# Optimization experiments

Hardware: AMD Instinct MI355X
Metric: run time of the kernel (lower is better)

Reference implementation:

```python
import jax, jax.numpy as jnp
import numpy as np

K = 3       # strip kernel taps
G = 2       # groups
PAD = (K - 1) // 2  # dilation=1


def setup_inputs() -> dict:
    key = jax.random.key(0)
    k1, k2, k3, k4, k5 = jax.random.split(key, 5)
    n, c, h, w = 8, 96, 256, 256
    x = jax.random.normal(k1, (n, c, h, w), dtype=jnp.float32)
    Wconv = jax.random.normal(k2, (G * K, c), dtype=jnp.float32) * 0.1   # 1x1 conv weight
    inside_all = jax.random.normal(k3, (c, 1, 1), dtype=jnp.float32) * 0.1
    lamb_l = jax.random.normal(k4, (c,), dtype=jnp.float32) * 0.1
    lamb_h = jax.random.normal(k5, (c,), dtype=jnp.float32) * 0.1
    return {"x": x, "Wconv": Wconv, "inside_all": inside_all,
            "lamb_l": lamb_l, "lamb_h": lamb_h}


def reference(x, Wconv, inside_all, lamb_l, lamb_h):
    n, c, h, w = x.shape
    cg = c // G
    # dynamic per-(sample, group) filter from global average pool + 1x1 conv + tanh
    m = x.mean(axis=(2, 3))                       # (n, c)
    filt = jnp.tanh(m @ Wconv.T).reshape(n, G, K)  # (n, G, K)
    # reflection pad along width (H=True -> horizontal strip)
    xp = jnp.pad(x, ((0, 0), (0, 0), (0, 0), (PAD, PAD)), mode="reflect")
    xr = xp.reshape(n, G, cg, h, w + 2 * PAD)
    # sliding-window multiply-accumulate over K taps (no unfold materialization)
    out = xr[..., 0:w] * filt[:, :, None, None, None, 0]
    for i in range(1, K):
        out = out + xr[..., i:i + w] * filt[:, :, None, None, None, i]
    out = out.reshape(n, c, h, w)
    # gated low/high residual mix; gap averages over width for H=True
    gap = x.mean(axis=3, keepdims=True)            # (n, c, h, 1)
    out_low = (out * (inside_all + 1.0) - inside_all * gap) * lamb_l[None, :, None, None]
    out_high = x * (lamb_h[None, :, None, None] + 1.0)
    return out_low + out_high
```

## Files before the change

kernel.cpp:

```cpp
#include <hip/hip_runtime.h>
#include <math.h>

#define NN 8
#define CC 96
#define HH 256
#define WW 256
#define GG 2
#define KK 3
#define CG (CC / GG)
#define HWD (HH * WW)

typedef float fvec4 __attribute__((ext_vector_type(4)));

__global__ __launch_bounds__(256) void mean_kernel(const float* __restrict__ x,
                                                   float* __restrict__ m) {
    const int b = blockIdx.x;
    const fvec4* xp = (const fvec4*)(x + (size_t)b * HWD);
    const int t = threadIdx.x;
    float s = 0.f;
#pragma unroll
    for (int i = 0; i < HWD / 4 / 256; ++i) {
        fvec4 v = xp[i * 256 + t];
        s += (v.x + v.y) + (v.z + v.w);
    }
#pragma unroll
    for (int off = 32; off; off >>= 1) s += __shfl_down(s, off, 64);
    __shared__ float ls[4];
    const int wid = t >> 6;
    if ((t & 63) == 0) ls[wid] = s;
    __syncthreads();
    if (t == 0) {
        float tot = (ls[0] + ls[1]) + (ls[2] + ls[3]);
        m[b] = tot * (1.0f / (float)HWD);
    }
}

__global__ void filt_kernel(const float* __restrict__ m,
                            const float* __restrict__ Wconv,
                            float* __restrict__ filt) {
    const int t = threadIdx.x;
    if (t >= NN * GG * KK) return;
    const int n = t / (GG * KK);
    const int gk = t % (GG * KK);
    float s = 0.f;
#pragma unroll
    for (int c = 0; c < CC; ++c) s += m[n * CC + c] * Wconv[gk * CC + c];
    filt[t] = tanhf(s);
}

__global__ __launch_bounds__(256) void main_kernel(
    const float* __restrict__ x, const float* __restrict__ filt,
    const float* __restrict__ inside_all, const float* __restrict__ lamb_l,
    const float* __restrict__ lamb_h, float* __restrict__ out) {
    const int wave = threadIdx.x >> 6;
    const int lane = threadIdx.x & 63;
    const int nc = blockIdx.x >> 6;
    const int row_in_nc = ((blockIdx.x & 63) << 2) + wave;
    const int c = nc % CC;
    const int n = nc / CC;
    const int g = c / CG;

    const float* fr = filt + (n * GG + g) * KK;
    const float f0 = fr[0], f1 = fr[1], f2 = fr[2];
    const float ia = inside_all[c];
    const float ll = lamb_l[c];
    const float lh1 = lamb_h[c] + 1.0f;

    const size_t base = ((size_t)nc * HH + row_in_nc) * WW;
    fvec4 v = ((const fvec4*)(x + base))[lane];

    float s = (v.x + v.y) + (v.z + v.w);
#pragma unroll
    for (int off = 1; off < 64; off <<= 1) s += __shfl_xor(s, off, 64);
    const float gap = s * (1.0f / (float)WW);

    const float left = __shfl_up(v.w, 1, 64);
    const float right = __shfl_down(v.x, 1, 64);
    const float xm1 = (lane == 0) ? v.y : left;
    const float xp1 = (lane == 63) ? v.z : right;

    const float c0 = f0 * xm1 + f1 * v.x + f2 * v.y;
    const float c1 = f0 * v.x + f1 * v.y + f2 * v.z;
    const float c2 = f0 * v.y + f1 * v.z + f2 * v.w;
    const float c3 = f0 * v.z + f1 * v.w + f2 * xp1;

    const float a = ia + 1.0f;
    const float bterm = ia * gap;

    fvec4 o;
    o.x = (c0 * a - bterm) * ll + v.x * lh1;
    o.y = (c1 * a - bterm) * ll + v.y * lh1;
    o.z = (c2 * a - bterm) * ll + v.z * lh1;
    o.w = (c3 * a - bterm) * ll + v.w * lh1;
    __builtin_nontemporal_store(o, (fvec4*)(out + base) + lane);
}

extern "C" void kernel_launch(void* const* d_in, const int* in_sizes, int n_in,
                              void* d_out, int out_size, void* d_ws,
                              size_t ws_size, hipStream_t stream) {
    const float* x = (const float*)d_in[0];
    const float* Wconv = (const float*)d_in[1];
    const float* inside_all = (const float*)d_in[2];
    const float* lamb_l = (const float*)d_in[3];
    const float* lamb_h = (const float*)d_in[4];
    float* out = (float*)d_out;

    float* m = (float*)d_ws;
    float* filt = m + NN * CC;

    mean_kernel<<<NN * CC, 256, 0, stream>>>(x, m);
    filt_kernel<<<1, 64, 0, stream>>>(m, Wconv, filt);
    main_kernel<<<(NN * CC * HH) / 4, 256, 0, stream>>>(x, filt, inside_all,
                                                        lamb_l, lamb_h, out);
}
```

Before: 92.68 us.

## Fuse mean, filter, and strip conv into one cooperative grid-synced kernel

Replaces the three-kernel sequence with a single cooperative kernel, one block per (n,c) plane. Each block first reduces its plane's sum, then waits at a grid-wide barrier, computes its 3-tap filter, and re-reads the plane in reverse row order so recently read rows may still be in cache. The aim is to remove two kernel launch gaps and part of the second HBM read of x. In exchange it adds a grid-sync barrier and a per-launch occupancy query, and it depends on all 768 blocks being co-resident.

New measurement: 247.9 us. 2.67x slower.

```diff
diff --git a/kernel.cpp b/kernel.cpp
--- a/kernel.cpp
+++ b/kernel.cpp
@@ -1,5 +1,8 @@
 #include <hip/hip_runtime.h>
+#include <hip/hip_cooperative_groups.h>
 #include <math.h>
+
+namespace cg = cooperative_groups;
 
 #define NN 8
 #define CC 96
@@ -7,10 +10,86 @@
 #define WW 256
 #define GG 2
 #define KK 3
-#define CG (CC / GG)
+#define CPG (CC / GG)
 #define HWD (HH * WW)
 
 typedef float fvec4 __attribute__((ext_vector_type(4)));
+
+__global__ __launch_bounds__(256, 4) void fused_kernel(
+    const float* __restrict__ x, const float* __restrict__ Wconv,
+    const float* __restrict__ inside_all, const float* __restrict__ lamb_l,
+    const float* __restrict__ lamb_h, float* __restrict__ out,
+    float* __restrict__ mp) {
+    const int nc = blockIdx.x;
+    const int t = threadIdx.x;
+    const int wave = t >> 6;
+    const int lane = t & 63;
+
+    const fvec4* xp = (const fvec4*)x + (size_t)nc * (HWD / 4);
+    float s = 0.f;
+#pragma unroll 8
+    for (int i = 0; i < HWD / 4 / 256; ++i) {
+        fvec4 v = xp[i * 256 + t];
+        s += (v.x + v.y) + (v.z + v.w);
+    }
+#pragma unroll
+    for (int off = 32; off; off >>= 1) s += __shfl_down(s, off, 64);
+    __shared__ float ls[4];
+    if (lane == 0) ls[wave] = s;
+    __syncthreads();
+    if (t == 0) mp[nc] = (ls[0] + ls[1]) + (ls[2] + ls[3]);
+    __threadfence();
+
+    cg::this_grid().sync();
+
+    const int c = nc % CC;
+    const int n = nc / CC;
+    const int g = c / CPG;
+    __shared__ float fsh[KK];
+    if (t < KK) {
+        const float* Wr = Wconv + (g * KK + t) * CC;
+        const float* p0 = mp + n * CC;
+        float acc = 0.f;
+#pragma unroll
+        for (int j = 0; j < CC; ++j) acc += p0[j] * Wr[j];
+        fsh[t] = tanhf(acc * (1.0f / (float)HWD));
+    }
+    __syncthreads();
+    const float f0 = fsh[0], f1 = fsh[1], f2 = fsh[2];
+    const float ia = inside_all[c];
+    const float ll = lamb_l[c];
+    const float lh1 = lamb_h[c] + 1.0f;
+    const float a = ia + 1.0f;
+
+    for (int r = HH / 4 - 1; r >= 0; --r) {
+        const int row = (r << 2) + wave;
+        const size_t base = ((size_t)nc * HH + row) * WW;
+        fvec4 v = ((const fvec4*)(x + base))[lane];
+
+        float rs = (v.x + v.y) + (v.z + v.w);
+#pragma unroll
+        for (int off = 1; off < 64; off <<= 1) rs += __shfl_xor(rs, off, 64);
+        const float gap = rs * (1.0f / (float)WW);
+
+        const float left = __shfl_up(v.w, 1, 64);
+        const float right = __shfl_down(v.x, 1, 64);
+        const float xm1 = (lane == 0) ? v.y : left;
+        const float xp1 = (lane == 63) ? v.z : right;
+
+        const float c0 = f0 * xm1 + f1 * v.x + f2 * v.y;
+        const float c1 = f0 * v.x + f1 * v.y + f2 * v.z;
+        const float c2 = f0 * v.y + f1 * v.z + f2 * v.w;
+        const float c3 = f0 * v.z + f1 * v.w + f2 * xp1;
+
+        const float bterm = ia * gap;
+        fvec4 o;
+        o.x = (c0 * a - bterm) * ll + v.x * lh1;
+        o.y = (c1 * a - bterm) * ll + v.y * lh1;
+        o.z = (c2 * a - bterm) * ll + v.z * lh1;
+        o.w = (c3 * a - bterm) * ll + v.w * lh1;
+        __builtin_nontemporal_store(o, (fvec4*)(out + base) + lane);
+    }
+}
 
 __global__ __launch_bounds__(256) void mean_kernel(const float* __restrict__ x,
                                                    float* __restrict__ m) {
@@ -18,7 +97,7 @@
     const fvec4* xp = (const fvec4*)(x + (size_t)b * HWD);
     const int t = threadIdx.x;
     float s = 0.f;
-#pragma unroll
+#pragma unroll 8
     for (int i = 0; i < HWD / 4 / 256; ++i) {
         fvec4 v = xp[i * 256 + t];
         s += (v.x + v.y) + (v.z + v.w);
@@ -29,10 +108,7 @@
     const int wid = t >> 6;
     if ((t & 63) == 0) ls[wid] = s;
     __syncthreads();
-    if (t == 0) {
-        float tot = (ls[0] + ls[1]) + (ls[2] + ls[3]);
-        m[b] = tot * (1.0f / (float)HWD);
-    }
+    if (t == 0) m[b] = ((ls[0] + ls[1]) + (ls[2] + ls[3])) * (1.0f / (float)HWD);
 }
 
 __global__ void filt_kernel(const float* __restrict__ m,
@@ -58,7 +134,7 @@
     const int row_in_nc = ((blockIdx.x & 63) << 2) + wave;
     const int c = nc % CC;
     const int n = nc / CC;
-    const int g = c / CG;
+    const int g = c / CPG;
 
     const float* fr = filt + (n * GG + g) * KK;
     const float f0 = fr[0], f1 = fr[1], f2 = fr[2];
@@ -104,12 +180,24 @@
     const float* lamb_l = (const float*)d_in[3];
     const float* lamb_h = (const float*)d_in[4];
     float* out = (float*)d_out;
-
-    float* m = (float*)d_ws;
-    float* filt = m + NN * CC;
-
-    mean_kernel<<<NN * CC, 256, 0, stream>>>(x, m);
-    filt_kernel<<<1, 64, 0, stream>>>(m, Wconv, filt);
-    main_kernel<<<(NN * CC * HH) / 4, 256, 0, stream>>>(x, filt, inside_all,
-                                                        lamb_l, lamb_h, out);
-}
+    float* mp = (float*)d_ws;
+
+    int maxblk = 0;
+    hipError_t qerr = hipOccupancyMaxActiveBlocksPerMultiprocessor(
+        &maxblk, fused_kernel, 256, 0);
+    const bool coop_ok = (qerr == hipSuccess) && (maxblk * 256 >= NN * CC);
+
+    if (coop_ok) {
+        void* kargs[] = {(void*)&x,      (void*)&Wconv, (void*)&inside_all,
+                         (void*)&lamb_l, (void*)&lamb_h, (void*)&out,
+                         (void*)&mp};
+        hipLaunchCooperativeKernel(fused_kernel, dim3(NN * CC), dim3(256),
+                                   kargs, 0, stream);
+    } else {
+        float* filt = mp + NN * CC;
+        mean_kernel<<<NN * CC, 256, 0, stream>>>(x, mp);
+        filt_kernel<<<1, 64, 0, stream>>>(mp, Wconv, filt);
+        main_kernel<<<(NN * CC * HH) / 4, 256, 0, stream>>>(
+            x, filt, inside_all, lamb_l, lamb_h, out);
+    }
+}
```

## Split mean reduction into chunks, fuse filter computation into main kernel, 4 rows/wave

Applied to the files above, without the earlier changes.

The per-channel mean is now computed as 8 partial sums per (n,c), which raises the reduction grid from 768 to 6144 blocks for better occupancy. The separate single-block filter kernel is removed. Each main-kernel block instead sums the partials for its sample and computes its group's 3 tanh filter taps in shared memory, which saves one launch and its serialization. Each wave now processes 4 rows instead of 1, so loads overlap and the extra per-block prologue is amortized, at the cost of redundant filter computation in every block.

Result: no change. 93.32 us (+0.7%).

```diff
diff --git a/kernel.cpp b/kernel.cpp
--- a/kernel.cpp
+++ b/kernel.cpp
@@ -7,92 +7,116 @@
 #define WW 256
 #define GG 2
 #define KK 3
-#define CG (CC / GG)
+#define CPG (CC / GG)
 #define HWD (HH * WW)
+#define CHUNKS 8
 
 typedef float fvec4 __attribute__((ext_vector_type(4)));
 
-__global__ __launch_bounds__(256) void mean_kernel(const float* __restrict__ x,
-                                                   float* __restrict__ m) {
+__global__ __launch_bounds__(256) void partial_kernel(
+    const float* __restrict__ x, float* __restrict__ mp) {
     const int b = blockIdx.x;
-    const fvec4* xp = (const fvec4*)(x + (size_t)b * HWD);
+    const int nc = b >> 3;
+    const int chunk = b & 7;
     const int t = threadIdx.x;
+    const fvec4* xp = (const fvec4*)x + (size_t)nc * (HWD / 4)
+                      + (size_t)chunk * (HWD / 4 / CHUNKS);
     float s = 0.f;
 #pragma unroll
-    for (int i = 0; i < HWD / 4 / 256; ++i) {
+    for (int i = 0; i < HWD / 4 / CHUNKS / 256; ++i) {
         fvec4 v = xp[i * 256 + t];
         s += (v.x + v.y) + (v.z + v.w);
     }
 #pragma unroll
     for (int off = 32; off; off >>= 1) s += __shfl_down(s, off, 64);
     __shared__ float ls[4];
-    const int wid = t >> 6;
-    if ((t & 63) == 0) ls[wid] = s;
+    if ((t & 63) == 0) ls[t >> 6] = s;
     __syncthreads();
-    if (t == 0) {
-        float tot = (ls[0] + ls[1]) + (ls[2] + ls[3]);
-        m[b] = tot * (1.0f / (float)HWD);
-    }
-}
-
-__global__ void filt_kernel(const float* __restrict__ m,
-                            const float* __restrict__ Wconv,
-                            float* __restrict__ filt) {
-    const int t = threadIdx.x;
-    if (t >= NN * GG * KK) return;
-    const int n = t / (GG * KK);
-    const int gk = t % (GG * KK);
-    float s = 0.f;
-#pragma unroll
-    for (int c = 0; c < CC; ++c) s += m[n * CC + c] * Wconv[gk * CC + c];
-    filt[t] = tanhf(s);
+    if (t == 0) mp[b] = (ls[0] + ls[1]) + (ls[2] + ls[3]);
 }
 
 __global__ __launch_bounds__(256) void main_kernel(
-    const float* __restrict__ x, const float* __restrict__ filt,
-    const float* __restrict__ inside_all, const float* __restrict__ lamb_l,
-    const float* __restrict__ lamb_h, float* __restrict__ out) {
-    const int wave = threadIdx.x >> 6;
-    const int lane = threadIdx.x & 63;
-    const int nc = blockIdx.x >> 6;
-    const int row_in_nc = ((blockIdx.x & 63) << 2) + wave;
+    const float* __restrict__ x, const float* __restrict__ mp,
+    const float* __restrict__ Wconv, const float* __restrict__ inside_all,
+    const float* __restrict__ lamb_l, const float* __restrict__ lamb_h,
+    float* __restrict__ out) {
+    const int bb = blockIdx.x;
+    const int nc = bb >> 4;
+    const int rblk = bb & 15;
+    const int t = threadIdx.x;
+    const int wave = t >> 6;
+    const int lane = t & 63;
     const int c = nc % CC;
     const int n = nc / CC;
-    const int g = c / CG;
+    const int g = c / CPG;
 
-    const float* fr = filt + (n * GG + g) * KK;
-    const float f0 = fr[0], f1 = fr[1], f2 = fr[2];
+    __shared__ float msh[CC];
+    __shared__ float fsh[KK];
+    if (t < CC) {
+        const float* pr = mp + ((size_t)n * CC + t) * CHUNKS;
+        float a0 = 0.f;
+#pragma unroll
+        for (int k = 0; k < CHUNKS; ++k) a0 += pr[k];
+        msh[t] = a0;
+    }
+    __syncthreads();
+    if (t < KK) {
+        const float* Wr = Wconv + (g * KK + t) * CC;
+        float acc = 0.f;
+#pragma unroll
+        for (int j = 0; j < CC; ++j) acc += msh[j] * Wr[j];
+        fsh[t] = tanhf(acc * (1.0f / (float)HWD));
+    }
+    __syncthreads();
+    const float f0 = fsh[0], f1 = fsh[1], f2 = fsh[2];
     const float ia = inside_all[c];
     const float ll = lamb_l[c];
     const float lh1 = lamb_h[c] + 1.0f;
+    const float a = ia + 1.0f;
 
-    const size_t base = ((size_t)nc * HH + row_in_nc) * WW;
-    fvec4 v = ((const fvec4*)(x + base))[lane];
+    const int row0 = (rblk << 4) + (wave << 2);
+    const size_t base = ((size_t)nc * HH + row0) * WW;
+    fvec4 v0 = ((const fvec4*)(x + base + 0 * WW))[lane];
+    fvec4 v1 = ((const fvec4*)(x + base + 1 * WW))[lane];
+    fvec4 v2 = ((const fvec4*)(x + base + 2 * WW))[lane];
+    fvec4 v3 = ((const fvec4*)(x + base + 3 * WW))[lane];
 
-    float s = (v.x + v.y) + (v.z + v.w);
+    float s0 = (v0.x + v0.y) + (v0.z + v0.w);
+    float s1 = (v1.x + v1.y) + (v1.z + v1.w);
+    float s2 = (v2.x + v2.y) + (v2.z + v2.w);
+    float s3 = (v3.x + v3.y) + (v3.z + v3.w);
 #pragma unroll
-    for (int off = 1; off < 64; off <<= 1) s += __shfl_xor(s, off, 64);
-    const float gap = s * (1.0f / (float)WW);
+    for (int off = 1; off < 64; off <<= 1) {
+        s0 += __shfl_xor(s0, off, 64);
+        s1 += __shfl_xor(s1, off, 64);
+        s2 += __shfl_xor(s2, off, 64);
+        s3 += __shfl_xor(s3, off, 64);
+    }
 
-    const float left = __shfl_up(v.w, 1, 64);
-    const float right = __shfl_down(v.x, 1, 64);
-    const float xm1 = (lane == 0) ? v.y : left;
-    const float xp1 = (lane == 63) ? v.z : right;
+#pragma unroll
+    for (int r = 0; r < 4; ++r) {
+        const fvec4 v = (r == 0) ? v0 : (r == 1) ? v1 : (r == 2) ? v2 : v3;
+        const float rs = (r == 0) ? s0 : (r == 1) ? s1 : (r == 2) ? s2 : s3;
+        const float gap = rs * (1.0f / (float)WW);
 
-    const float c0 = f0 * xm1 + f1 * v.x + f2 * v.y;
-    const float c1 = f0 * v.x + f1 * v.y + f2 * v.z;
-    const float c2 = f0 * v.y + f1 * v.z + f2 * v.w;
-    const float c3 = f0 * v.z + f1 * v.w + f2 * xp1;
+        const float left = __shfl_up(v.w, 1, 64);
+        const float right = __shfl_down(v.x, 1, 64);
+        const float xm1 = (lane == 0) ? v.y : left;
+        const float xp1 = (lane == 63) ? v.z : right;
 
-    const float a = ia + 1.0f;
-    const float bterm = ia * gap;
+        const float c0 = f0 * xm1 + f1 * v.x + f2 * v.y;
+        const float c1 = f0 * v.x + f1 * v.y + f2 * v.z;
+        const float c2 = f0 * v.y + f1 * v.z + f2 * v.w;
+        const float c3 = f0 * v.z + f1 * v.w + f2 * xp1;
 
-    fvec4 o;
-    o.x = (c0 * a - bterm) * ll + v.x * lh1;
-    o.y = (c1 * a - bterm) * ll + v.y * lh1;
-    o.z = (c2 * a - bterm) * ll + v.z * lh1;
-    o.w = (c3 * a - bterm) * ll + v.w * lh1;
-    __builtin_nontemporal_store(o, (fvec4*)(out + base) + lane);
+        const float bterm = ia * gap;
+        fvec4 o;
+        o.x = (c0 * a - bterm) * ll + v.x * lh1;
+        o.y = (c1 * a - bterm) * ll + v.y * lh1;
+        o.z = (c2 * a - bterm) * ll + v.z * lh1;
+        o.w = (c3 * a - bterm) * ll + v.w * lh1;
+        __builtin_nontemporal_store(o, (fvec4*)(out + base + r * WW) + lane);
+    }
 }
 
 extern "C" void kernel_launch(void* const* d_in, const int* in_sizes, int n_in,
@@ -104,12 +128,9 @@
     const float* lamb_l = (const float*)d_in[3];
     const float* lamb_h = (const float*)d_in[4];
     float* out = (float*)d_out;
+    float* mp = (float*)d_ws;
 
-    float* m = (float*)d_ws;
-    float* filt = m + NN * CC;
-
-    mean_kernel<<<NN * CC, 256, 0, stream>>>(x, m);
-    filt_kernel<<<1, 64, 0, stream>>>(m, Wconv, filt);
-    main_kernel<<<(NN * CC * HH) / 4, 256, 0, stream>>>(x, filt, inside_all,
-                                                        lamb_l, lamb_h, out);
+    partial_kernel<<<NN * CC * CHUNKS, 256, 0, stream>>>(x, mp);
+    main_kernel<<<NN * CC * (HH / 16), 256, 0, stream>>>(
+        x, mp, Wconv, inside_all, lamb_l, lamb_h, out);
 }
```
